# Performance work log

Measured on AMD Instinct MI355X. Metric: run time of the kernel, lower is better.

## Reference

```python
import jax, jax.numpy as jnp
import numpy as np
from jax import lax

B, C, H, W = 64, 3, 256, 256
E, D = 64, 32          # expert_nums, embed_dim
TOP_K = 2
NOISE_EPS = 0.01
ALPHA = 0.8


def setup_inputs() -> dict:
    key = jax.random.key(0)
    ks = jax.random.split(key, 16)
    n = lambda k, shape, s=0.05: jax.random.normal(k, shape, jnp.float32) * s
    return {
        "task_id": jax.random.randint(ks[0], (B,), 0, 10),
        "degradation_info": jax.random.normal(ks[1], (B, C, H, W), jnp.float32),
        "noise": jax.random.normal(ks[2], (B, E), jnp.float32),
        "mlp_w1": n(ks[3], (1, D)), "mlp_b1": jnp.zeros((D,), jnp.float32),
        "mlp_w2": n(ks[4], (D, D)), "mlp_b2": jnp.zeros((D,), jnp.float32),
        "conv1_w": n(ks[5], (16, C, 3, 3)), "conv1_b": jnp.zeros((16,), jnp.float32),
        "conv2_w": n(ks[6], (32, 16, 3, 3)), "conv2_b": jnp.zeros((32,), jnp.float32),
        "deg_w": n(ks[7], (32, D)), "deg_b": jnp.zeros((D,), jnp.float32),
        "expert_keys": jax.random.normal(ks[8], (E, D), jnp.float32),
        "gate_w": n(ks[9], (E, E)), "gate_b": jnp.zeros((E,), jnp.float32),
        "noise_w": n(ks[10], (E, E)), "noise_b": jnp.zeros((E,), jnp.float32),
    }


def _conv(x, w):
    return lax.conv_general_dilated(
        x, w, window_strides=(1, 1), padding="SAME",
        dimension_numbers=("NCHW", "OIHW", "NCHW"))


def reference(task_id, degradation_info, noise,
              mlp_w1, mlp_b1, mlp_w2, mlp_b2,
              conv1_w, conv1_b, conv2_w, conv2_b,
              deg_w, deg_b, expert_keys,
              gate_w, gate_b, noise_w, noise_b):
    # task embedding: Linear(1,D) -> ReLU -> Linear(D,D)
    t = task_id.astype(jnp.float32)[:, None]                       # [B,1]
    task_embed = jax.nn.relu(t @ mlp_w1 + mlp_b1) @ mlp_w2 + mlp_b2  # [B,D]

    # degradation conv embed: conv->relu->conv->relu->global avg pool
    h = jax.nn.relu(_conv(degradation_info, conv1_w) + conv1_b[None, :, None, None])
    h = jax.nn.relu(_conv(h, conv2_w) + conv2_b[None, :, None, None])
    feat = h.mean(axis=(2, 3))                                     # [B,32]
    deg_embed = feat @ deg_w + deg_b                               # [B,D]

    combined = task_embed + (1.0 - ALPHA) * deg_embed              # [B,D]
    sim = combined @ expert_keys.T / jnp.sqrt(jnp.float32(D))      # [B,E]
    expert_weight = jax.nn.softmax(sim, axis=1)

    clean_logits = expert_weight @ gate_w + gate_b                 # [B,E]
    stddev = jax.nn.softplus(expert_weight @ noise_w + noise_b) + NOISE_EPS
    logits = clean_logits + noise * stddev                         # train=True path

    top_logits, top_idx = lax.top_k(logits, min(TOP_K + 1, E))
    tk_logits = top_logits[:, :TOP_K]                              # [B,k]
    tk_idx = top_idx[:, :TOP_K]
    tk_gates = jax.nn.softmax(tk_logits, axis=1)

    rows = jnp.arange(logits.shape[0])[:, None]
    gates = jnp.zeros_like(logits).at[rows, tk_idx].set(tk_gates)  # scatter
    load = gates.sum(axis=0)                                       # [E]
    return gates, load
```

## Files before the change

kernel.cpp:

```cpp
#include <hip/hip_runtime.h>
#include <math.h>

typedef __attribute__((ext_vector_type(8)))  short  short8;
typedef __attribute__((ext_vector_type(4)))  float  floatx4;
typedef __attribute__((ext_vector_type(16))) float  floatx16;
typedef __attribute__((ext_vector_type(2)))  float  floatx2;

__device__ inline short bf16rne(float f) {
    unsigned u = __float_as_uint(f);
    unsigned r = (u + 0x7FFFu + ((u >> 16) & 1u)) >> 16;
    return (short)r;
}
__device__ inline unsigned pack2bf(float a, float b) {
    return (unsigned)(unsigned short)bf16rne(a) |
           ((unsigned)(unsigned short)bf16rne(b) << 16);
}

#define WS_FRAG_OFF 8192
#define WS_BIAS_OFF (8192 + 10 * 64 * 16)

__global__ __launch_bounds__(256) void build_frags_kernel(
    const float* __restrict__ w1,
    const float* __restrict__ b1,
    const float* __restrict__ w2,
    const float* __restrict__ b2,
    void* __restrict__ ws,
    float* __restrict__ out)
{
    const int t = threadIdx.x;
    float* feat = (float*)ws;
    for (int i = t; i < 2048; i += 256) feat[i] = 0.0f;
    if (t >= 64 && t < 128) out[4096 + (t - 64)] = 0.0f;

    if (t < 64) {
        const int lane = t;
        const int q = lane >> 4, ml = lane & 15;
        const int n32 = lane & 31, half = lane >> 5;
        short8* F = (short8*)((char*)ws + WS_FRAG_OFF);
        floatx2* Bv = (floatx2*)((char*)ws + WS_BIAS_OFF);

        short8 B1;
#pragma unroll
        for (int j = 0; j < 8; ++j) {
            int k = q * 8 + j;
            B1[j] = (k < 27) ? bf16rne(w1[ml * 27 + k]) : (short)0;
        }
        F[lane] = B1;

#pragma unroll
        for (int s = 0; s < 9; ++s) {
            short8 Bs;
#pragma unroll
            for (int j = 0; j < 8; ++j) {
                int ic = half * 8 + j;
                Bs[j] = bf16rne(w2[(n32 * 16 + ic) * 9 + s]);
            }
            F[(1 + s) * 64 + lane] = Bs;
        }
        floatx2 bb; bb.x = b1[ml]; bb.y = b2[n32];
        Bv[lane] = bb;
    }
}

__global__ __launch_bounds__(256, 4) void conv_feat_kernel(
    const float* __restrict__ x,
    const void*  __restrict__ ws_ro,
    float* __restrict__ feat_sum)
{
    __shared__ short s_in[3 * 20 * 24];
    __shared__ short s_h1[324 * 24];
    __shared__ float s_part[4][32];

    const int t    = threadIdx.x;
    const int lane = t & 63, wv = t >> 6;
    const int q    = lane >> 4, ml = lane & 15;
    const int n32  = lane & 31, half = lane >> 5;
    const int tx = blockIdx.x, ty = blockIdx.y, b = blockIdx.z;
    const bool border = (tx == 0) | (tx == 15) | (ty == 0) | (ty == 15);

    const short8* F = (const short8*)((const char*)ws_ro + WS_FRAG_OFF);
    short8 B1 = F[lane];
    short8 B2[9];
#pragma unroll
    for (int s = 0; s < 9; ++s) B2[s] = F[(1 + s) * 64 + lane];
    floatx2 bias = ((const floatx2*)((const char*)ws_ro + WS_BIAS_OFF))[lane];

    int lc[8];
#pragma unroll
    for (int j = 0; j < 8; ++j) {
        int k = q * 8 + j;
        int kk = (k < 27) ? k : 0;
        int c = kk / 9, s = kk % 9;
        lc[j] = (c * 480 + (s / 3) * 24 + (s % 3)) * 2;
    }
    const bool q3 = (q == 3);

    const int gy0 = ty * 16 - 2, gx0 = tx * 16 - 2;
    const float* xb = x + (size_t)b * 3 * 65536;
    if (!border) {
        for (int i = t; i < 600; i += 256) {
            int c = i / 200, rem = i % 200, r = rem / 10, c2 = rem % 10;
            const float* p = xb + c * 65536 + (gy0 + r) * 256 + gx0 + 2 * c2;
            floatx2 v = *(const floatx2*)p;
            *(unsigned*)&s_in[(c * 20 + r) * 24 + 2 * c2] = pack2bf(v.x, v.y);
        }
    } else {
        for (int i = t; i < 600; i += 256) {
            int c = i / 200, rem = i % 200, r = rem / 10, c2 = rem % 10;
            int gy = gy0 + r, gx = gx0 + 2 * c2;
            float v0 = 0.0f, v1 = 0.0f;
            if ((unsigned)gy < 256u) {
                const float* p = xb + c * 65536 + gy * 256;
                if ((unsigned)gx < 256u)       v0 = p[gx];
                if ((unsigned)(gx + 1) < 256u) v1 = p[gx + 1];
            }
            *(unsigned*)&s_in[(c * 20 + r) * 24 + 2 * c2] = pack2bf(v0, v1);
        }
    }
    __syncthreads();

#pragma unroll
    for (int i = 0; i < 5; ++i) {
        int tile = wv + 4 * i;
        int p = tile * 16 + ml;
        int iy = p / 18, ix = p % 18;
        int pixb = (iy * 24 + ix) * 2;
        short8 A;
#pragma unroll
        for (int j = 0; j < 8; ++j)
            A[j] = *(const short*)((const char*)s_in + pixb + lc[j]);
        if (q3) { A[3] = 0; A[4] = 0; A[5] = 0; A[6] = 0; A[7] = 0; }
        floatx4 acc = {0.f, 0.f, 0.f, 0.f};
        acc = __builtin_amdgcn_mfma_f32_16x16x32_bf16(A, B1, acc, 0, 0, 0);
        int p20 = tile * 16 + q * 4;
        int hb = p20 * 24 + ml;
        if (!border) {
#pragma unroll
            for (int r = 0; r < 4; ++r)
                s_h1[hb + r * 24] = bf16rne(fmaxf(acc[r] + bias.x, 0.0f));
        } else {
#pragma unroll
            for (int r = 0; r < 4; ++r) {
                int p2 = p20 + r;
                int iy2 = p2 / 18, ix2 = p2 % 18;
                int gy = ty * 16 - 1 + iy2, gx = tx * 16 - 1 + ix2;
                float v = fmaxf(acc[r] + bias.x, 0.0f);
                if (!((unsigned)gy < 256u && (unsigned)gx < 256u)) v = 0.0f;
                s_h1[hb + r * 24] = bf16rne(v);
            }
        }
    }
    if (wv == 0) {
        int p = 320 + ml; if (p > 323) p = 323;
        int iy = p / 18, ix = p % 18;
        int pixb = (iy * 24 + ix) * 2;
        short8 A;
#pragma unroll
        for (int j = 0; j < 8; ++j)
            A[j] = *(const short*)((const char*)s_in + pixb + lc[j]);
        if (q3) { A[3] = 0; A[4] = 0; A[5] = 0; A[6] = 0; A[7] = 0; }
        floatx4 acc = {0.f, 0.f, 0.f, 0.f};
        acc = __builtin_amdgcn_mfma_f32_16x16x32_bf16(A, B1, acc, 0, 0, 0);
        if (q == 0) {
#pragma unroll
            for (int r = 0; r < 4; ++r) {
                int p2 = 320 + r;
                int iy2 = p2 / 18, ix2 = p2 % 18;
                int gy = ty * 16 - 1 + iy2, gx = tx * 16 - 1 + ix2;
                float v = fmaxf(acc[r] + bias.x, 0.0f);
                if (!((unsigned)gy < 256u && (unsigned)gx < 256u)) v = 0.0f;
                s_h1[p2 * 24 + ml] = bf16rne(v);
            }
        }
    }
    __syncthreads();

    float part = 0.0f;
#pragma unroll
    for (int tt = 0; tt < 2; ++tt) {
        int tl = 2 * wv + tt;
        int prow = 2 * tl + (n32 >> 4);
        int pcol = n32 & 15;
        const short* base = &s_h1[(prow * 18 + pcol) * 24 + half * 8];
        floatx16 acc = {0.f,0.f,0.f,0.f,0.f,0.f,0.f,0.f,
                        0.f,0.f,0.f,0.f,0.f,0.f,0.f,0.f};
#pragma unroll
        for (int s = 0; s < 9; ++s) {
            int ky = s / 3, kx = s % 3;
            short8 A = *(const short8*)(base + (ky * 18 + kx) * 24);
            acc = __builtin_amdgcn_mfma_f32_32x32x16_bf16(A, B2[s], acc, 0, 0, 0);
        }
#pragma unroll
        for (int r = 0; r < 16; ++r) part += fmaxf(acc[r] + bias.y, 0.0f);
    }
    part += __shfl_xor(part, 32);
    if (lane < 32) s_part[wv][n32] = part;
    __syncthreads();
    if (t < 32) {
        float ssum = s_part[0][t] + s_part[1][t] + s_part[2][t] + s_part[3][t];
        atomicAdd(feat_sum + b * 32 + t, ssum);
    }
}

__global__ __launch_bounds__(64) void router_gate_kernel(
    const int* __restrict__ task_id,
    const float* __restrict__ noise,
    const float* __restrict__ mlp_w1,
    const float* __restrict__ mlp_b1,
    const float* __restrict__ mlp_w2,
    const float* __restrict__ mlp_b2,
    const float* __restrict__ deg_w,
    const float* __restrict__ deg_b,
    const float* __restrict__ keys,
    const float* __restrict__ gate_w,
    const float* __restrict__ gate_b,
    const float* __restrict__ noise_w,
    const float* __restrict__ noise_b,
    const float* __restrict__ feat_sum,
    float* __restrict__ out)
{
    const int b = blockIdx.x;
    const int e = threadIdx.x;

    __shared__ float s_te[32];
    __shared__ float s_comb[32];
    __shared__ float s_ew[64];

    if (e < 32) {
        float tf = (float)task_id[b];
        s_te[e] = fmaxf(tf * mlp_w1[e] + mlp_b1[e], 0.0f);
    }
    __syncthreads();
    if (e < 32) {
        float acc = mlp_b2[e];
        for (int k = 0; k < 32; ++k) acc += s_te[k] * mlp_w2[k * 32 + e];
        float dacc = deg_b[e];
        for (int c = 0; c < 32; ++c)
            dacc += (feat_sum[b * 32 + c] * (1.0f / 65536.0f)) * deg_w[c * 32 + e];
        s_comb[e] = acc + 0.2f * dacc;
    }
    __syncthreads();

    float s = 0.0f;
    for (int d = 0; d < 32; ++d) s += s_comb[d] * keys[e * 32 + d];
    s *= 0.17677669529663687f;

    float m = s;
    for (int off = 32; off; off >>= 1) m = fmaxf(m, __shfl_xor(m, off));
    float p = expf(s - m);
    float sum = p;
    for (int off = 32; off; off >>= 1) sum += __shfl_xor(sum, off);
    float w = p / sum;
    s_ew[e] = w;
    __syncthreads();

    float cl = gate_b[e], nz = noise_b[e];
    for (int k = 0; k < 64; ++k) {
        float ewk = s_ew[k];
        cl += ewk * gate_w[k * 64 + e];
        nz += ewk * noise_w[k * 64 + e];
    }
    float sp = (nz > 20.0f) ? nz : log1pf(expf(nz));
    float logit = cl + noise[b * 64 + e] * (sp + 0.01f);

    float v0 = logit; int i0 = e;
    for (int off = 32; off; off >>= 1) {
        float ov = __shfl_xor(v0, off);
        int   oi = __shfl_xor(i0, off);
        if (ov > v0 || (ov == v0 && oi < i0)) { v0 = ov; i0 = oi; }
    }
    float v1 = (e == i0) ? -INFINITY : logit; int i1 = e;
    for (int off = 32; off; off >>= 1) {
        float ov = __shfl_xor(v1, off);
        int   oi = __shfl_xor(i1, off);
        if (ov > v1 || (ov == v1 && oi < i1)) { v1 = ov; i1 = oi; }
    }

    float e1 = expf(v1 - v0);
    float g0 = 1.0f / (1.0f + e1);
    float g1 = e1 / (1.0f + e1);

    float g = (e == i0) ? g0 : (e == i1) ? g1 : 0.0f;
    out[b * 64 + e] = g;
    if (g != 0.0f) atomicAdd(out + 64 * 64 + e, g);
}

extern "C" void kernel_launch(void* const* d_in, const int* in_sizes, int n_in,
                              void* d_out, int out_size, void* d_ws, size_t ws_size,
                              hipStream_t stream) {
    const int*   task_id = (const int*)d_in[0];
    const float* x       = (const float*)d_in[1];
    const float* noise   = (const float*)d_in[2];
    const float* mlp_w1  = (const float*)d_in[3];
    const float* mlp_b1  = (const float*)d_in[4];
    const float* mlp_w2  = (const float*)d_in[5];
    const float* mlp_b2  = (const float*)d_in[6];
    const float* conv1_w = (const float*)d_in[7];
    const float* conv1_b = (const float*)d_in[8];
    const float* conv2_w = (const float*)d_in[9];
    const float* conv2_b = (const float*)d_in[10];
    const float* deg_w   = (const float*)d_in[11];
    const float* deg_b   = (const float*)d_in[12];
    const float* keys    = (const float*)d_in[13];
    const float* gate_w  = (const float*)d_in[14];
    const float* gate_b  = (const float*)d_in[15];
    const float* noise_w = (const float*)d_in[16];
    const float* noise_b = (const float*)d_in[17];

    float* out  = (float*)d_out;
    float* feat = (float*)d_ws;

    build_frags_kernel<<<1, 256, 0, stream>>>(conv1_w, conv1_b, conv2_w,
                                              conv2_b, d_ws, out);
    dim3 gridA(16, 16, 64);
    conv_feat_kernel<<<gridA, 256, 0, stream>>>(x, d_ws, feat);
    router_gate_kernel<<<64, 64, 0, stream>>>(
        task_id, noise, mlp_w1, mlp_b1, mlp_w2, mlp_b2, deg_w, deg_b, keys,
        gate_w, gate_b, noise_w, noise_b, feat, out);
}
```

Before: 205.8 us.

## Swizzle conv1 output layout, fold biases into MFMA accumulators, use packed bf16 conversion

Conv1 now swaps its MFMA operands so each lane holds four consecutive channels of one pixel. Those are packed into a single 8-byte LDS store, with an XOR swizzle on even and odd pixels to cut bank conflicts. Conv2 reads with the matching swizzle, and both biases are preloaded into the accumulators so the separate adds go away. The patch also uses the hardware packed bf16 convert when it is available, splits the border and interior paths, and raises the occupancy hint to 6 waves. The risk is higher register pressure at the larger occupancy target and extra index arithmetic.

```diff
diff --git a/kernel.cpp b/kernel.cpp
--- a/kernel.cpp
+++ b/kernel.cpp
@@ -5,19 +5,27 @@
 typedef __attribute__((ext_vector_type(4)))  float  floatx4;
 typedef __attribute__((ext_vector_type(16))) float  floatx16;
 typedef __attribute__((ext_vector_type(2)))  float  floatx2;
-
-__device__ inline short bf16rne(float f) {
+typedef __attribute__((ext_vector_type(2)))  unsigned uintx2;
+
+__device__ __forceinline__ short bf16rne(float f) {
     unsigned u = __float_as_uint(f);
     unsigned r = (u + 0x7FFFu + ((u >> 16) & 1u)) >> 16;
     return (short)r;
 }
-__device__ inline unsigned pack2bf(float a, float b) {
+
+__device__ __forceinline__ unsigned pk2(float a, float b) {
+#if __has_builtin(__builtin_amdgcn_cvt_pk_bf16_f32)
+    auto t = __builtin_amdgcn_cvt_pk_bf16_f32(a, b);
+    unsigned u; __builtin_memcpy(&u, &t, 4); return u;
+#else
     return (unsigned)(unsigned short)bf16rne(a) |
            ((unsigned)(unsigned short)bf16rne(b) << 16);
-}
-
-#define WS_FRAG_OFF 8192
-#define WS_BIAS_OFF (8192 + 10 * 64 * 16)
+#endif
+}
+
+#define WS_FRAG_OFF  8192
+#define WS_BIAS1_OFF (WS_FRAG_OFF + 10 * 64 * 16)
+#define WS_BIAS2_OFF (WS_BIAS1_OFF + 64 * 16)
 
 __global__ __launch_bounds__(256) void build_frags_kernel(
     const float* __restrict__ w1,
@@ -37,15 +45,14 @@
         const int q = lane >> 4, ml = lane & 15;
         const int n32 = lane & 31, half = lane >> 5;
         short8* F = (short8*)((char*)ws + WS_FRAG_OFF);
-        floatx2* Bv = (floatx2*)((char*)ws + WS_BIAS_OFF);
-
-        short8 B1;
+
+        short8 W1;
 #pragma unroll
         for (int j = 0; j < 8; ++j) {
             int k = q * 8 + j;
-            B1[j] = (k < 27) ? bf16rne(w1[ml * 27 + k]) : (short)0;
-        }
-        F[lane] = B1;
+            W1[j] = (k < 27) ? bf16rne(w1[ml * 27 + k]) : (short)0;
+        }
+        F[lane] = W1;
 
 #pragma unroll
         for (int s = 0; s < 9; ++s) {
@@ -57,12 +64,33 @@
             }
             F[(1 + s) * 64 + lane] = Bs;
         }
-        floatx2 bb; bb.x = b1[ml]; bb.y = b2[n32];
-        Bv[lane] = bb;
-    }
-}
-
-__global__ __launch_bounds__(256, 4) void conv_feat_kernel(
+        floatx4 bv;
+#pragma unroll
+        for (int r = 0; r < 4; ++r) bv[r] = b1[q * 4 + r];
+        ((floatx4*)((char*)ws + WS_BIAS1_OFF))[lane] = bv;
+        ((float*)((char*)ws + WS_BIAS2_OFF))[lane] = b2[n32];
+    }
+}
+
+__device__ __forceinline__ void conv1_tile(
+    short* __restrict__ s_h1, const short* __restrict__ s_in,
+    const int* lcS, int gOff, int wIdx, bool valid, bool q3,
+    short8 W1, floatx4 biasv)
+{
+    short8 Bx;
+#pragma unroll
+    for (int j = 0; j < 8; ++j) Bx[j] = s_in[gOff + lcS[j]];
+    if (q3) { Bx[3] = 0; Bx[4] = 0; Bx[5] = 0; Bx[6] = 0; Bx[7] = 0; }
+    floatx4 acc = biasv;
+    acc = __builtin_amdgcn_mfma_f32_16x16x32_bf16(W1, Bx, acc, 0, 0, 0);
+    float v0 = fmaxf(acc[0], 0.f), v1 = fmaxf(acc[1], 0.f);
+    float v2 = fmaxf(acc[2], 0.f), v3 = fmaxf(acc[3], 0.f);
+    if (!valid) { v0 = 0.f; v1 = 0.f; v2 = 0.f; v3 = 0.f; }
+    uintx2 w; w.x = pk2(v0, v1); w.y = pk2(v2, v3);
+    *(uintx2*)&s_h1[wIdx] = w;
+}
+
+__global__ __launch_bounds__(256, 6) void conv_feat_kernel(
     const float* __restrict__ x,
     const void*  __restrict__ ws_ro,
     float* __restrict__ feat_sum)
@@ -79,21 +107,23 @@
     const bool border = (tx == 0) | (tx == 15) | (ty == 0) | (ty == 15);
 
     const short8* F = (const short8*)((const char*)ws_ro + WS_FRAG_OFF);
-    short8 B1 = F[lane];
+    short8 W1 = F[lane];
     short8 B2[9];
 #pragma unroll
     for (int s = 0; s < 9; ++s) B2[s] = F[(1 + s) * 64 + lane];
-    floatx2 bias = ((const floatx2*)((const char*)ws_ro + WS_BIAS_OFF))[lane];
-
-    int lc[8];
+    floatx4 biasv = ((const floatx4*)((const char*)ws_ro + WS_BIAS1_OFF))[lane];
+    float   b2v   = ((const float*)((const char*)ws_ro + WS_BIAS2_OFF))[lane];
+
+    int lcS[8];
 #pragma unroll
     for (int j = 0; j < 8; ++j) {
         int k = q * 8 + j;
         int kk = (k < 27) ? k : 0;
         int c = kk / 9, s = kk % 9;
-        lc[j] = (c * 480 + (s / 3) * 24 + (s % 3)) * 2;
+        lcS[j] = (c * 20 + s / 3) * 24 + (s % 3);
     }
     const bool q3 = (q == 3);
+    const int swz1 = (q * 4) ^ ((ml & 1) * 8);
 
     const int gy0 = ty * 16 - 2, gx0 = tx * 16 - 2;
     const float* xb = x + (size_t)b * 3 * 65536;
@@ -102,7 +132,7 @@
             int c = i / 200, rem = i % 200, r = rem / 10, c2 = rem % 10;
             const float* p = xb + c * 65536 + (gy0 + r) * 256 + gx0 + 2 * c2;
             floatx2 v = *(const floatx2*)p;
-            *(unsigned*)&s_in[(c * 20 + r) * 24 + 2 * c2] = pack2bf(v.x, v.y);
+            *(unsigned*)&s_in[(c * 20 + r) * 24 + 2 * c2] = pk2(v.x, v.y);
         }
     } else {
         for (int i = t; i < 600; i += 256) {
@@ -114,84 +144,90 @@
                 if ((unsigned)gx < 256u)       v0 = p[gx];
                 if ((unsigned)(gx + 1) < 256u) v1 = p[gx + 1];
             }
-            *(unsigned*)&s_in[(c * 20 + r) * 24 + 2 * c2] = pack2bf(v0, v1);
-        }
-    }
-    __syncthreads();
-
-#pragma unroll
-    for (int i = 0; i < 5; ++i) {
-        int tile = wv + 4 * i;
-        int p = tile * 16 + ml;
-        int iy = p / 18, ix = p % 18;
-        int pixb = (iy * 24 + ix) * 2;
-        short8 A;
-#pragma unroll
-        for (int j = 0; j < 8; ++j)
-            A[j] = *(const short*)((const char*)s_in + pixb + lc[j]);
-        if (q3) { A[3] = 0; A[4] = 0; A[5] = 0; A[6] = 0; A[7] = 0; }
-        floatx4 acc = {0.f, 0.f, 0.f, 0.f};
-        acc = __builtin_amdgcn_mfma_f32_16x16x32_bf16(A, B1, acc, 0, 0, 0);
-        int p20 = tile * 16 + q * 4;
-        int hb = p20 * 24 + ml;
-        if (!border) {
-#pragma unroll
-            for (int r = 0; r < 4; ++r)
-                s_h1[hb + r * 24] = bf16rne(fmaxf(acc[r] + bias.x, 0.0f));
+            *(unsigned*)&s_in[(c * 20 + r) * 24 + 2 * c2] = pk2(v0, v1);
+        }
+    }
+    __syncthreads();
+
+    if (!border) {
+#pragma unroll
+        for (int i = 0; i < 4; ++i) {
+            int tile = wv + 4 * i;
+            conv1_tile(s_h1, s_in, lcS, ml + tile * 24,
+                       (tile * 18 + ml) * 24 + swz1, true, q3, W1, biasv);
+        }
+        int t4 = wv + 16;
+        if (wv < 2) {
+            conv1_tile(s_h1, s_in, lcS, ml + t4 * 24,
+                       (t4 * 18 + ml) * 24 + swz1, true, q3, W1, biasv);
         } else {
-#pragma unroll
-            for (int r = 0; r < 4; ++r) {
-                int p2 = p20 + r;
-                int iy2 = p2 / 18, ix2 = p2 % 18;
-                int gy = ty * 16 - 1 + iy2, gx = tx * 16 - 1 + ix2;
-                float v = fmaxf(acc[r] + bias.x, 0.0f);
-                if (!((unsigned)gy < 256u && (unsigned)gx < 256u)) v = 0.0f;
-                s_h1[hb + r * 24] = bf16rne(v);
-            }
-        }
-    }
-    if (wv == 0) {
-        int p = 320 + ml; if (p > 323) p = 323;
-        int iy = p / 18, ix = p % 18;
-        int pixb = (iy * 24 + ix) * 2;
-        short8 A;
-#pragma unroll
-        for (int j = 0; j < 8; ++j)
-            A[j] = *(const short*)((const char*)s_in + pixb + lc[j]);
-        if (q3) { A[3] = 0; A[4] = 0; A[5] = 0; A[6] = 0; A[7] = 0; }
-        floatx4 acc = {0.f, 0.f, 0.f, 0.f};
-        acc = __builtin_amdgcn_mfma_f32_16x16x32_bf16(A, B1, acc, 0, 0, 0);
-        if (q == 0) {
-#pragma unroll
-            for (int r = 0; r < 4; ++r) {
-                int p2 = 320 + r;
-                int iy2 = p2 / 18, ix2 = p2 % 18;
-                int gy = ty * 16 - 1 + iy2, gx = tx * 16 - 1 + ix2;
-                float v = fmaxf(acc[r] + bias.x, 0.0f);
-                if (!((unsigned)gy < 256u && (unsigned)gx < 256u)) v = 0.0f;
-                s_h1[p2 * 24 + ml] = bf16rne(v);
-            }
+            int cc = wv - 2;
+            conv1_tile(s_h1, s_in, lcS, ml * 24 + 16 + cc,
+                       (ml * 18 + 16 + cc) * 24 + ((q * 4) ^ (cc * 8)),
+                       true, q3, W1, biasv);
+        }
+        if (wv == 0) {
+            int ml2 = ml & 3;
+            int iy = 16 + (ml2 >> 1), ix = 16 + (ml2 & 1);
+            conv1_tile(s_h1, s_in, lcS, iy * 24 + ix,
+                       (iy * 18 + ix) * 24 + ((q * 4) ^ ((ml2 & 1) * 8)),
+                       true, q3, W1, biasv);
+        }
+    } else {
+        const bool gxOK = (unsigned)(tx * 16 - 1 + ml) < 256u;
+#pragma unroll
+        for (int i = 0; i < 4; ++i) {
+            int tile = wv + 4 * i;
+            bool rowOK = (unsigned)(ty * 16 - 1 + tile) < 256u;
+            conv1_tile(s_h1, s_in, lcS, ml + tile * 24,
+                       (tile * 18 + ml) * 24 + swz1, rowOK & gxOK, q3, W1, biasv);
+        }
+        int t4 = wv + 16;
+        if (wv < 2) {
+            bool rowOK = (unsigned)(ty * 16 - 1 + t4) < 256u;
+            conv1_tile(s_h1, s_in, lcS, ml + t4 * 24,
+                       (t4 * 18 + ml) * 24 + swz1, rowOK & gxOK, q3, W1, biasv);
+        } else {
+            int cc = wv - 2;
+            bool ok = ((unsigned)(ty * 16 - 1 + ml) < 256u) &
+                      ((unsigned)(tx * 16 + 15 + cc) < 256u);
+            conv1_tile(s_h1, s_in, lcS, ml * 24 + 16 + cc,
+                       (ml * 18 + 16 + cc) * 24 + ((q * 4) ^ (cc * 8)),
+                       ok, q3, W1, biasv);
+        }
+        if (wv == 0) {
+            int ml2 = ml & 3;
+            int iy = 16 + (ml2 >> 1), ix = 16 + (ml2 & 1);
+            bool ok = ((unsigned)(ty * 16 - 1 + iy) < 256u) &
+                      ((unsigned)(tx * 16 - 1 + ix) < 256u);
+            conv1_tile(s_h1, s_in, lcS, iy * 24 + ix,
+                       (iy * 18 + ix) * 24 + ((q * 4) ^ ((ml2 & 1) * 8)),
+                       ok, q3, W1, biasv);
         }
     }
     __syncthreads();
 
     float part = 0.0f;
+    const int prow0 = (n32 >> 4), pcol = n32 & 15;
+    const int sw  = (half * 8) ^ ((n32 & 1) * 8);
+    const int swX = sw ^ 8;
 #pragma unroll
     for (int tt = 0; tt < 2; ++tt) {
-        int tl = 2 * wv + tt;
-        int prow = 2 * tl + (n32 >> 4);
-        int pcol = n32 & 15;
-        const short* base = &s_h1[(prow * 18 + pcol) * 24 + half * 8];
-        floatx16 acc = {0.f,0.f,0.f,0.f,0.f,0.f,0.f,0.f,
-                        0.f,0.f,0.f,0.f,0.f,0.f,0.f,0.f};
+        int pix0 = (2 * (2 * wv + tt) + prow0) * 18 + pcol;
+        const short* A0 = s_h1 + pix0 * 24 + sw;
+        const short* A1 = s_h1 + pix0 * 24 + swX;
+        floatx16 acc;
+#pragma unroll
+        for (int r = 0; r < 16; ++r) acc[r] = b2v;
 #pragma unroll
         for (int s = 0; s < 9; ++s) {
-            int ky = s / 3, kx = s % 3;
-            short8 A = *(const short8*)(base + (ky * 18 + kx) * 24);
-            acc = __builtin_amdgcn_mfma_f32_32x32x16_bf16(A, B2[s], acc, 0, 0, 0);
-        }
-#pragma unroll
-        for (int r = 0; r < 16; ++r) part += fmaxf(acc[r] + bias.y, 0.0f);
+            const int ky = s / 3, kx = s % 3;
+            const short* p = ((kx & 1) ? A1 : A0) + (ky * 18 + kx) * 24;
+            short8 Ax = *(const short8*)p;
+            acc = __builtin_amdgcn_mfma_f32_32x32x16_bf16(Ax, B2[s], acc, 0, 0, 0);
+        }
+#pragma unroll
+        for (int r = 0; r < 16; ++r) part += fmaxf(acc[r], 0.0f);
     }
     part += __shfl_xor(part, 32);
     if (lane < 32) s_part[wv][n32] = part;
```

Result: faster. 199.0 us (-3.3%).
